# Optimization experiments

Measured on AMD Instinct MI355X. Metric: run time of the kernel, lower is better.

Reference implementation:

```python
import jax, jax.numpy as jnp
import numpy as np

B, QH, QW = 16, 64, 64
KH, KW = 64, 64
H, D, DK, K, S = 8, 256, 32, 4, 1


def setup_inputs() -> dict:
    key = jax.random.key(0)
    ks = jax.random.split(key, 16)
    def lin(i, din, dout, wscale=1.0):
        w = jax.random.normal(ks[i], (din, dout), jnp.float32) * (wscale / np.sqrt(din))
        b = jax.random.normal(ks[i + 1], (dout,), jnp.float32) * 0.02
        return w, b
    Wq, bq = lin(0, D, D)
    Wb, bb = lin(2, D, D)
    Wk, bk = lin(4, D, D)
    Woff, boff = lin(6, D, 2 * H * K * S, wscale=0.1)  # small offsets keep samples near ref point
    WA, bA = lin(8, D, H * K * S)
    Wm, bm = lin(10, D, D)
    return dict(
        query=jax.random.normal(ks[12], (B, QH, QW, D), jnp.float32),
        keys=jax.random.normal(ks[13], (B, KH, KW, D), jnp.float32),
        ref_point=jax.random.uniform(ks[14], (B, QH, QW, 2), jnp.float32),
        src_query=jax.random.normal(ks[15], (B, QH, QW, D), jnp.float32),
        Wq=Wq, bq=bq, Wb=Wb, bb=bb, Wk=Wk, bk=bk,
        Woff=Woff, boff=boff, WA=WA, bA=bA, Wm=Wm, bm=bm)


def _bilinear_zeros(img, px, py):
    # img [N, Hs, Ws, C]; px, py pixel coords [N, K, QH, QW]
    # Matches torch F.grid_sample(mode='bilinear', padding_mode='zeros'):
    # each out-of-bounds corner contributes zero.
    N, Hs, Ws, _ = img.shape
    x0 = jnp.floor(px); y0 = jnp.floor(py)
    wx1 = px - x0; wy1 = py - y0
    n = jnp.arange(N)[:, None, None, None]
    def corner(xf, yf, w):
        xi = xf.astype(jnp.int32); yi = yf.astype(jnp.int32)
        valid = (xi >= 0) & (xi < Ws) & (yi >= 0) & (yi < Hs)
        v = img[n, jnp.clip(yi, 0, Hs - 1), jnp.clip(xi, 0, Ws - 1)]
        return v * (w * valid)[..., None]
    return (corner(x0, y0, (1 - wx1) * (1 - wy1)) + corner(x0 + 1, y0, wx1 * (1 - wy1))
            + corner(x0, y0 + 1, (1 - wx1) * wy1) + corner(x0 + 1, y0 + 1, wx1 * wy1))


def reference(query, keys, ref_point, src_query, Wq, bq, Wb, bb, Wk, bk,
              Woff, boff, WA, bA, Wm, bm):
    _ = query @ Wq + bq  # q_proj output is computed but unused in the original forward
    sq = src_query @ Wb + bb
    off = (sq @ Woff + boff).reshape(B, QH, QW, H, S, K, 2)
    off = off.transpose(0, 3, 4, 5, 1, 2, 6).reshape(B * H, S, K, QH, QW, 2)
    A = jax.nn.softmax((sq @ WA + bA).reshape(B, QH, QW, H, S * K), axis=-1)
    A = A.transpose(0, 3, 1, 2, 4).reshape(B * H, QH, QW, S, K)
    # k_proj on the (single-scale) key feature map -> per-head maps [B*H, KH, KW, DK]
    kf = (keys @ Wk + bk).reshape(B, KH, KW, H, DK).transpose(0, 3, 1, 2, 4).reshape(B * H, KH, KW, DK)
    # restore_scale then torch .repeat(h,1,1,1): flat index n -> batch n % B (faithful to original)
    rr = ref_point * jnp.array([KW - 1, KH - 1], jnp.float32)
    rr = jnp.tile(rr, (H, 1, 1, 1))  # [B*H, QH, QW, 2]
    samples = []
    for l in range(S):
        pts = rr[:, None] + off[:, l]                 # [B*H, K, QH, QW, 2]
        vgx = 2.0 * pts[..., 0] / max(KW - 1, 1) - 1.0
        vgy = 2.0 * pts[..., 1] / max(KH - 1, 1) - 1.0
        px = ((vgx + 1.0) * KW - 1.0) / 2.0           # grid_sample align_corners=False unnormalize
        py = ((vgy + 1.0) * KH - 1.0) / 2.0
        samples.append(_bilinear_zeros(kf, px, py))   # [B*H, K, QH, QW, DK]
    samp = jnp.stack(samples, axis=1)                 # [B*H, S, K, QH, QW, DK]
    feat = jnp.einsum('nskhwd,nhwsk->nhwd', samp, A)  # weighted sum over scales*points
    feat = feat.reshape(B, H, QH, QW, DK).transpose(0, 2, 3, 1, 4).reshape(B, QH, QW, D)
    return feat @ Wm + bm
```

## Files before the change

kernel.cpp:

```cpp
#include <hip/hip_runtime.h>
#include <hip/hip_bf16.h>

using bf16 = __hip_bfloat16;
typedef short bf16x8 __attribute__((ext_vector_type(8)));
typedef float f32x4 __attribute__((ext_vector_type(4)));

#define DD 256
#define MTOT 65536

static __device__ __forceinline__ short f2bs(float f) {
    bf16 h = __float2bfloat16(f);
    return *reinterpret_cast<short*>(&h);
}
static __device__ __forceinline__ float bs2f(short s) {
    unsigned u = (unsigned)(unsigned short)s << 16;
    return __uint_as_float(u);
}

static __device__ __forceinline__ void gll16(const void* g, void* l) {
    __builtin_amdgcn_global_load_lds(
        (const __attribute__((address_space(1))) unsigned int*)g,
        (__attribute__((address_space(3))) unsigned int*)l, 16, 0, 0);
}

static __device__ __forceinline__ int swz_idx(int n, int k) {
    return n * 256 + ((((k >> 3) ^ (n & 7)) << 3) | (k & 7));
}

__global__ __launch_bounds__(256) void k_transpose(
    const float* __restrict__ Wb, const float* __restrict__ Wk, const float* __restrict__ Wm,
    const float* __restrict__ Woff, const float* __restrict__ WA,
    bf16* __restrict__ WbT, bf16* __restrict__ WkT, bf16* __restrict__ WmT,
    bf16* __restrict__ WoffAT)
{
    int idx = blockIdx.x * 256 + threadIdx.x;
    if (idx < 3 * 65536) {
        int which = idx >> 16, e = idx & 65535;
        int i = e >> 8, j = e & 255;
        const float* src = which == 0 ? Wb : (which == 1 ? Wk : Wm);
        bf16*        dst = which == 0 ? WbT : (which == 1 ? WkT : WmT);
        dst[swz_idx(j, i)] = __float2bfloat16(src[e]);
    } else {
        int e = idx - 3 * 65536;
        if (e < 96 * 256) {
            int j = e >> 8, i = e & 255;
            WoffAT[swz_idx(j, i)] = __float2bfloat16((j < 64) ? Woff[i * 64 + j]
                                                              : WA[i * 32 + (j - 64)]);
        }
    }
}

template <int NTW, int NCOLS, bool AF32>
static __device__ __forceinline__ void gemm_lds2(
    const void* __restrict__ Av, const bf16* __restrict__ BTswz,
    bf16* __restrict__ Bs, char* __restrict__ As,
    int row0, int tid, f32x4 (&acc)[2][NTW])
{
    const int wave = tid >> 6, lane = tid & 63;
    const int rg = wave >> 1, cg = wave & 1;
    const int rsub = lane & 15, kg = lane >> 4;
    constexpr int SB = NCOLS / 32;
    constexpr int SA = AF32 ? 4 : 2;
    constexpr int ABYTES = AF32 ? 16384 : 8192;

    auto stageB = [&](int s) {
#pragma unroll
        for (int i = 0; i < SB; ++i) {
            int cc = wave * SB + i;
            int i16 = cc * 64 + lane;
            int n = i16 >> 3, lg = i16 & 7;
            gll16(BTswz + (size_t)n * 256 + s * 64 + lg * 8, (char*)Bs + (size_t)i16 * 16);
        }
    };
    auto stageA = [&](int s, int buf) {
#pragma unroll
        for (int i = 0; i < SA; ++i) {
            if constexpr (AF32) {
                int cc = wave * 4 + i;
                int row = cc * 4 + (lane >> 4);
                int g = (lane & 15) ^ (row & 15);
                gll16((const float*)Av + (size_t)(row0 + row) * DD + s * 64 + g * 4,
                      As + (size_t)buf * ABYTES + cc * 1024 + lane * 16);
            } else {
                int cc = wave * 2 + i;
                int row = cc * 8 + (lane >> 3);
                int g = (lane & 7) ^ (row & 7);
                gll16((const bf16*)Av + (size_t)(row0 + row) * DD + s * 64 + g * 8,
                      As + (size_t)buf * ABYTES + cc * 1024 + lane * 16);
            }
        }
    };

    stageA(0, 0);
    int cur = 0;
#pragma unroll
    for (int s = 0; s < 4; ++s) {
        stageB(s);
        if (s < 3) {
            stageA(s + 1, cur ^ 1);
            asm volatile("s_waitcnt vmcnt(%0)" :: "i"(SA) : "memory");
        } else {
            asm volatile("s_waitcnt vmcnt(0)" ::: "memory");
        }
        __builtin_amdgcn_s_barrier();
#pragma unroll
        for (int kkl = 0; kkl < 2; ++kkl) {
            bf16x8 afr[2];
#pragma unroll
            for (int st = 0; st < 2; ++st) {
                int row = rg * 32 + st * 16 + rsub;
                if constexpr (AF32) {
                    const char* base = As + cur * ABYTES + row * 256;
                    int G0 = kkl * 8 + kg * 2;
                    f32x4 v0 = *(const f32x4*)(base + ((G0 ^ (row & 15)) << 4));
                    f32x4 v1 = *(const f32x4*)(base + (((G0 + 1) ^ (row & 15)) << 4));
                    bf16x8 a;
#pragma unroll
                    for (int e = 0; e < 4; ++e) { a[e] = f2bs(v0[e]); a[e + 4] = f2bs(v1[e]); }
                    afr[st] = a;
                } else {
                    const char* base = As + cur * ABYTES + row * 128;
                    int g = kkl * 4 + kg;
                    afr[st] = *(const bf16x8*)(base + ((g ^ (row & 7)) << 4));
                }
            }
            int lg = kkl * 4 + kg;
#pragma unroll
            for (int nt = 0; nt < NTW; ++nt) {
                int n = cg * (NTW * 16) + nt * 16 + rsub;
                bf16x8 b = *(const bf16x8*)((const char*)Bs + (size_t)n * 128 + ((lg ^ (n & 7)) << 4));
                acc[0][nt] = __builtin_amdgcn_mfma_f32_16x16x32_bf16(afr[0], b, acc[0][nt], 0, 0, 0);
                acc[1][nt] = __builtin_amdgcn_mfma_f32_16x16x32_bf16(afr[1], b, acc[1][nt], 0, 0, 0);
            }
        }
        asm volatile("s_waitcnt lgkmcnt(0)" ::: "memory");
        __builtin_amdgcn_s_barrier();
        cur ^= 1;
    }
}

__global__ __launch_bounds__(256) void k_gemm_sqoffA(
    const float* __restrict__ src, const bf16* __restrict__ WbT, const float* __restrict__ bb,
    const bf16* __restrict__ WoffAT, const float* __restrict__ boff, const float* __restrict__ bA,
    float* __restrict__ off_ws, float* __restrict__ A_ws)
{
    __shared__ __align__(16) bf16 Bs[256 * 64];
    __shared__ __align__(16) char As[2 * 16384];
    int tid = threadIdx.x, lane = tid & 63, wave = tid >> 6;
    int row0 = blockIdx.x * 64;
    f32x4 acc[2][8] = {};
    gemm_lds2<8, 256, true>(src, WbT, Bs, As, row0, tid, acc);

    {
        int col = lane & 15;
        int jbase = (wave & 1) * 128;
        int lrb = (wave >> 1) * 32 + ((lane >> 4) << 2);
#pragma unroll
        for (int mt = 0; mt < 2; ++mt)
#pragma unroll
            for (int nt = 0; nt < 8; ++nt) {
                int j = jbase + nt * 16 + col;
                float bias = bb[j];
                int g = j >> 3;
#pragma unroll
                for (int r = 0; r < 4; ++r) {
                    int lr = lrb + mt * 16 + r;
                    *(short*)(As + lr * 512 + (((g ^ (lr & 7)) << 4)) + (j & 7) * 2) =
                        f2bs(acc[mt][nt][r] + bias);
                }
            }
    }
    __syncthreads();

    f32x4 acc2[2][3] = {};
    const int rsub = lane & 15, kg = lane >> 4;
    const int rg = wave >> 1, cg2 = wave & 1;
    auto stageOB = [&](int s, int buf) {
#pragma unroll
        for (int i = 0; i < 3; ++i) {
            int i16 = (wave * 3 + i) * 64 + lane;
            int n = i16 >> 3, lg = i16 & 7;
            gll16(WoffAT + (size_t)n * 256 + s * 64 + lg * 8,
                  (char*)Bs + buf * 12288 + (size_t)i16 * 16);
        }
    };
    stageOB(0, 0);
    int cur = 0;
#pragma unroll
    for (int s = 0; s < 4; ++s) {
        if (s < 3) {
            stageOB(s + 1, cur ^ 1);
            asm volatile("s_waitcnt vmcnt(3)" ::: "memory");
        } else {
            asm volatile("s_waitcnt vmcnt(0)" ::: "memory");
        }
        __builtin_amdgcn_s_barrier();
#pragma unroll
        for (int kkl = 0; kkl < 2; ++kkl) {
            bf16x8 afr[2];
#pragma unroll
            for (int st = 0; st < 2; ++st) {
                int lr = rg * 32 + st * 16 + rsub;
                int g = s * 8 + kkl * 4 + kg;
                afr[st] = *(const bf16x8*)(As + lr * 512 + ((g ^ (lr & 7)) << 4));
            }
            int lg = kkl * 4 + kg;
#pragma unroll
            for (int nt = 0; nt < 3; ++nt) {
                int n = cg2 * 48 + nt * 16 + rsub;
                bf16x8 b = *(const bf16x8*)((const char*)Bs + cur * 12288 + (size_t)n * 128
                                            + ((lg ^ (n & 7)) << 4));
                acc2[0][nt] = __builtin_amdgcn_mfma_f32_16x16x32_bf16(afr[0], b, acc2[0][nt], 0, 0, 0);
                acc2[1][nt] = __builtin_amdgcn_mfma_f32_16x16x32_bf16(afr[1], b, acc2[1][nt], 0, 0, 0);
            }
        }
        asm volatile("s_waitcnt lgkmcnt(0)" ::: "memory");
        __builtin_amdgcn_s_barrier();
        cur ^= 1;
    }
    int col = lane & 15;
    int jbase = cg2 * 48;
    int rb = row0 + rg * 32 + ((lane >> 4) << 2);
#pragma unroll
    for (int mt = 0; mt < 2; ++mt) {
#pragma unroll
        for (int nt = 0; nt < 3; ++nt) {
            int j = jbase + nt * 16 + col;
            if (j < 64) {
                float bias = boff[j];
#pragma unroll
                for (int r = 0; r < 4; ++r) {
                    int m = rb + mt * 16 + r;
                    off_ws[(size_t)m * 64 + j] = acc2[mt][nt][r] + bias;
                }
            } else {
                int ac = j - 64;
                float bias = bA[ac];
#pragma unroll
                for (int r = 0; r < 4; ++r) {
                    int m = rb + mt * 16 + r;
                    float v  = acc2[mt][nt][r] + bias;
                    float mx = fmaxf(v, __shfl_xor(v, 1));
                    mx       = fmaxf(mx, __shfl_xor(mx, 2));
                    float e  = __expf(v - mx);
                    float su = e + __shfl_xor(e, 1);
                    su      += __shfl_xor(su, 2);
                    A_ws[(size_t)m * 32 + ac] = e / su;
                }
            }
        }
    }
}

__global__ __launch_bounds__(256) void k_gemm_kf(
    const float* __restrict__ keys, const bf16* __restrict__ WkT,
    const float* __restrict__ bk, bf16* __restrict__ kf)
{
    __shared__ __align__(16) bf16 Bs[256 * 64];
    __shared__ __align__(16) char As[2 * 16384];
    int tid = threadIdx.x, lane = tid & 63, wave = tid >> 6;
    int row0 = blockIdx.x * 64;
    f32x4 acc[2][8] = {};
    gemm_lds2<8, 256, true>(keys, WkT, Bs, As, row0, tid, acc);
    int col = lane & 15;
    int jbase = (wave & 1) * 128;
    int rb = row0 + (wave >> 1) * 32 + ((lane >> 4) << 2);
#pragma unroll
    for (int mt = 0; mt < 2; ++mt)
#pragma unroll
        for (int nt = 0; nt < 8; ++nt) {
            int j = jbase + nt * 16 + col;
            float bias = bk[j];
#pragma unroll
            for (int r = 0; r < 4; ++r) {
                int m = rb + mt * 16 + r;
                size_t dst = (((size_t)(m >> 12) * 8 + (j >> 5)) * 4096 + (m & 4095)) * 32 + (j & 31);
                kf[dst] = __float2bfloat16(acc[mt][nt][r] + bias);
            }
        }
}

__global__ __launch_bounds__(256) void k_sample(
    const float* __restrict__ ref_point, const float* __restrict__ off_ws,
    const float* __restrict__ A_ws, const bf16* __restrict__ kf,
    bf16* __restrict__ feat)
{
    int bid = blockIdx.x;
    int xcd = bid & 7, within = bid >> 3;
    int bb_ = xcd * 2 + (within >> 9);
    int pixblk = within & 511;
    int t  = threadIdx.x;
    int q  = t >> 5;
    int h  = (t >> 2) & 7;
    int cg = t & 3;
    int m  = (bb_ << 12) + pixblk * 8 + q;
    int b  = bb_, pix = m & 4095;
    int rbatch = (b * 8 + h) & 15;
    const float* rp = ref_point + ((size_t)rbatch * 4096 + pix) * 2;
    float rx = rp[0] * 63.0f;
    float ry = rp[1] * 63.0f;
    const bf16* kfh = kf + ((size_t)(b * 8 + h) * 4096) * 32 + cg * 8;
    float acc[8] = {};
#pragma unroll
    for (int k = 0; k < 4; ++k) {
        const float* op = off_ws + (size_t)m * 64 + (h * 4 + k) * 2;
        float ox = op[0], oy = op[1];
        float a  = A_ws[(size_t)m * 32 + h * 4 + k];
        float px = (rx + ox) * (64.0f / 63.0f) - 0.5f;
        float py = (ry + oy) * (64.0f / 63.0f) - 0.5f;
        float x0 = floorf(px), y0 = floorf(py);
        float wx1 = px - x0, wy1 = py - y0;
        int xi = (int)x0, yi = (int)y0;
        float ax0 = (1.f - wx1) * ((xi     >= 0 && xi     < 64) ? 1.f : 0.f);
        float ax1 = wx1         * ((xi + 1 >= 0 && xi + 1 < 64) ? 1.f : 0.f);
        float ay0 = (1.f - wy1) * ((yi     >= 0 && yi     < 64) ? a : 0.f);
        float ay1 = wy1         * ((yi + 1 >= 0 && yi + 1 < 64) ? a : 0.f);
        int xc0 = min(max(xi, 0), 63),      xc1 = min(max(xi + 1, 0), 63);
        int yc0 = min(max(yi, 0), 63) * 64, yc1 = min(max(yi + 1, 0), 63) * 64;
        bf16x8 v00 = *(const bf16x8*)(kfh + (yc0 + xc0) * 32);
        bf16x8 v01 = *(const bf16x8*)(kfh + (yc0 + xc1) * 32);
        bf16x8 v10 = *(const bf16x8*)(kfh + (yc1 + xc0) * 32);
        bf16x8 v11 = *(const bf16x8*)(kfh + (yc1 + xc1) * 32);
        float w00 = ax0 * ay0, w01 = ax1 * ay0, w10 = ax0 * ay1, w11 = ax1 * ay1;
#pragma unroll
        for (int e = 0; e < 8; ++e) {
            acc[e] += w00 * bs2f(v00[e]) + w01 * bs2f(v01[e])
                    + w10 * bs2f(v10[e]) + w11 * bs2f(v11[e]);
        }
    }
    bf16x8 o;
#pragma unroll
    for (int e = 0; e < 8; ++e) o[e] = f2bs(acc[e]);
    *(bf16x8*)(feat + (size_t)m * DD + h * 32 + cg * 8) = o;
}

__global__ __launch_bounds__(256) void k_gemm_out(
    const bf16* __restrict__ feat, const bf16* __restrict__ WmT,
    const float* __restrict__ bm, float* __restrict__ out)
{
    __shared__ __align__(16) bf16 Bs[256 * 64];
    __shared__ __align__(16) char As[2 * 8192];
    int tid = threadIdx.x, lane = tid & 63, wave = tid >> 6;
    int row0 = blockIdx.x * 64;
    f32x4 acc[2][8] = {};
    gemm_lds2<8, 256, false>(feat, WmT, Bs, As, row0, tid, acc);
    int col = lane & 15;
    int jbase = (wave & 1) * 128;
    int rb = row0 + (wave >> 1) * 32 + ((lane >> 4) << 2);
#pragma unroll
    for (int mt = 0; mt < 2; ++mt)
#pragma unroll
        for (int nt = 0; nt < 8; ++nt) {
            int j = jbase + nt * 16 + col;
            float bias = bm[j];
#pragma unroll
            for (int r = 0; r < 4; ++r)
                out[(size_t)(rb + mt * 16 + r) * DD + j] =
                    acc[mt][nt][r] + bias;
        }
}

extern "C" void kernel_launch(void* const* d_in, const int* in_sizes, int n_in,
                              void* d_out, int out_size, void* d_ws, size_t ws_size,
                              hipStream_t stream)
{
    (void)in_sizes; (void)n_in; (void)out_size; (void)ws_size;
    const float* keys = (const float*)d_in[1];
    const float* refp = (const float*)d_in[2];
    const float* srcq = (const float*)d_in[3];
    const float* Wb   = (const float*)d_in[6];
    const float* bb   = (const float*)d_in[7];
    const float* Wk   = (const float*)d_in[8];
    const float* bk   = (const float*)d_in[9];
    const float* Woff = (const float*)d_in[10];
    const float* boff = (const float*)d_in[11];
    const float* WA   = (const float*)d_in[12];
    const float* bA   = (const float*)d_in[13];
    const float* Wm   = (const float*)d_in[14];
    const float* bm   = (const float*)d_in[15];

    char* ws = (char*)d_ws;
    bf16*  WbT    = (bf16*)(ws + 0);
    bf16*  WkT    = (bf16*)(ws + 131072);
    bf16*  WmT    = (bf16*)(ws + 262144);
    bf16*  WoffAT = (bf16*)(ws + 393216);
    bf16*  kf_ws  = (bf16*)(ws + 442368 + 33554432ull);
    bf16*  feat_ws= (bf16*)(ws + 442368 + 2ull * 33554432ull);
    float* off_ws = (float*)(ws + 442368 + 3ull * 33554432ull);
    float* A_ws   = (float*)(ws + 442368 + 3ull * 33554432ull + 16777216ull);

    float* out = (float*)d_out;

    k_transpose  <<<864, 256, 0, stream>>>(Wb, Wk, Wm, Woff, WA, WbT, WkT, WmT, WoffAT);
    k_gemm_sqoffA<<<1024, 256, 0, stream>>>(srcq, WbT, bb, WoffAT, boff, bA, off_ws, A_ws);
    k_gemm_kf    <<<1024, 256, 0, stream>>>(keys, WkT, bk, kf_ws);
    k_sample     <<<8192, 256, 0, stream>>>(refp, off_ws, A_ws, kf_ws, feat_ws);
    k_gemm_out   <<<1024, 256, 0, stream>>>(feat_ws, WmT, bm, out);
}
```

Baseline: 122.6 us.

## Fuse sampling into output GEMM and merge the two projection GEMMs

Merges the sq/off/A GEMM and the key-projection GEMM into one launch, with interleaved blocks dispatched by block-index parity over shared LDS. Fuses bilinear sampling with the output projection: each block samples 64 rows straight into a swizzled LDS A-tile, then runs the MFMA GEMM against Wm. This drops the feat workspace round-trip and two launches. In exchange the sample stage now runs with 1024 blocks instead of 8192, which lowers latency hiding for the gather loads, and 64KB of LDS per block may limit occupancy.

```diff
diff --git a/kernel.cpp b/kernel.cpp
--- a/kernel.cpp
+++ b/kernel.cpp
@@ -139,15 +139,16 @@
     }
 }
 
-__global__ __launch_bounds__(256) void k_gemm_sqoffA(
+static __device__ void body_sqoffA(
+    int bid, char* smem,
     const float* __restrict__ src, const bf16* __restrict__ WbT, const float* __restrict__ bb,
     const bf16* __restrict__ WoffAT, const float* __restrict__ boff, const float* __restrict__ bA,
     float* __restrict__ off_ws, float* __restrict__ A_ws)
 {
-    __shared__ __align__(16) bf16 Bs[256 * 64];
-    __shared__ __align__(16) char As[2 * 16384];
+    bf16* Bs = (bf16*)smem;
+    char* As = smem + 32768;
     int tid = threadIdx.x, lane = tid & 63, wave = tid >> 6;
-    int row0 = blockIdx.x * 64;
+    int row0 = bid * 64;
     f32x4 acc[2][8] = {};
     gemm_lds2<8, 256, true>(src, WbT, Bs, As, row0, tid, acc);
 
@@ -252,14 +253,15 @@
     }
 }
 
-__global__ __launch_bounds__(256) void k_gemm_kf(
+static __device__ void body_kf(
+    int bid, char* smem,
     const float* __restrict__ keys, const bf16* __restrict__ WkT,
     const float* __restrict__ bk, bf16* __restrict__ kf)
 {
-    __shared__ __align__(16) bf16 Bs[256 * 64];
-    __shared__ __align__(16) char As[2 * 16384];
+    bf16* Bs = (bf16*)smem;
+    char* As = smem + 32768;
     int tid = threadIdx.x, lane = tid & 63, wave = tid >> 6;
-    int row0 = blockIdx.x * 64;
+    int row0 = bid * 64;
     f32x4 acc[2][8] = {};
     gemm_lds2<8, 256, true>(keys, WkT, Bs, As, row0, tid, acc);
     int col = lane & 15;
@@ -280,73 +282,121 @@
         }
 }
 
-__global__ __launch_bounds__(256) void k_sample(
+__global__ __launch_bounds__(256) void k_fusedA(
+    const float* __restrict__ src, const bf16* __restrict__ WbT, const float* __restrict__ bb,
+    const bf16* __restrict__ WoffAT, const float* __restrict__ boff, const float* __restrict__ bA,
+    float* __restrict__ off_ws, float* __restrict__ A_ws,
+    const float* __restrict__ keys, const bf16* __restrict__ WkT,
+    const float* __restrict__ bk, bf16* __restrict__ kf)
+{
+    __shared__ __align__(16) char smem[65536];
+    int bid = blockIdx.x;
+    if (bid & 1)
+        body_kf(bid >> 1, smem, keys, WkT, bk, kf);
+    else
+        body_sqoffA(bid >> 1, smem, src, WbT, bb, WoffAT, boff, bA, off_ws, A_ws);
+}
+
+__global__ __launch_bounds__(256) void k_sample_out(
     const float* __restrict__ ref_point, const float* __restrict__ off_ws,
     const float* __restrict__ A_ws, const bf16* __restrict__ kf,
-    bf16* __restrict__ feat)
-{
-    int bid = blockIdx.x;
-    int xcd = bid & 7, within = bid >> 3;
-    int bb_ = xcd * 2 + (within >> 9);
-    int pixblk = within & 511;
-    int t  = threadIdx.x;
-    int q  = t >> 5;
-    int h  = (t >> 2) & 7;
-    int cg = t & 3;
-    int m  = (bb_ << 12) + pixblk * 8 + q;
-    int b  = bb_, pix = m & 4095;
-    int rbatch = (b * 8 + h) & 15;
-    const float* rp = ref_point + ((size_t)rbatch * 4096 + pix) * 2;
-    float rx = rp[0] * 63.0f;
-    float ry = rp[1] * 63.0f;
-    const bf16* kfh = kf + ((size_t)(b * 8 + h) * 4096) * 32 + cg * 8;
-    float acc[8] = {};
-#pragma unroll
-    for (int k = 0; k < 4; ++k) {
-        const float* op = off_ws + (size_t)m * 64 + (h * 4 + k) * 2;
-        float ox = op[0], oy = op[1];
-        float a  = A_ws[(size_t)m * 32 + h * 4 + k];
-        float px = (rx + ox) * (64.0f / 63.0f) - 0.5f;
-        float py = (ry + oy) * (64.0f / 63.0f) - 0.5f;
-        float x0 = floorf(px), y0 = floorf(py);
-        float wx1 = px - x0, wy1 = py - y0;
-        int xi = (int)x0, yi = (int)y0;
-        float ax0 = (1.f - wx1) * ((xi     >= 0 && xi     < 64) ? 1.f : 0.f);
-        float ax1 = wx1         * ((xi + 1 >= 0 && xi + 1 < 64) ? 1.f : 0.f);
-        float ay0 = (1.f - wy1) * ((yi     >= 0 && yi     < 64) ? a : 0.f);
-        float ay1 = wy1         * ((yi + 1 >= 0 && yi + 1 < 64) ? a : 0.f);
-        int xc0 = min(max(xi, 0), 63),      xc1 = min(max(xi + 1, 0), 63);
-        int yc0 = min(max(yi, 0), 63) * 64, yc1 = min(max(yi + 1, 0), 63) * 64;
-        bf16x8 v00 = *(const bf16x8*)(kfh + (yc0 + xc0) * 32);
-        bf16x8 v01 = *(const bf16x8*)(kfh + (yc0 + xc1) * 32);
-        bf16x8 v10 = *(const bf16x8*)(kfh + (yc1 + xc0) * 32);
-        bf16x8 v11 = *(const bf16x8*)(kfh + (yc1 + xc1) * 32);
-        float w00 = ax0 * ay0, w01 = ax1 * ay0, w10 = ax0 * ay1, w11 = ax1 * ay1;
-#pragma unroll
-        for (int e = 0; e < 8; ++e) {
-            acc[e] += w00 * bs2f(v00[e]) + w01 * bs2f(v01[e])
-                    + w10 * bs2f(v10[e]) + w11 * bs2f(v11[e]);
-        }
-    }
-    bf16x8 o;
-#pragma unroll
-    for (int e = 0; e < 8; ++e) o[e] = f2bs(acc[e]);
-    *(bf16x8*)(feat + (size_t)m * DD + h * 32 + cg * 8) = o;
-}
-
-__global__ __launch_bounds__(256) void k_gemm_out(
-    const bf16* __restrict__ feat, const bf16* __restrict__ WmT,
-    const float* __restrict__ bm, float* __restrict__ out)
-{
-    __shared__ __align__(16) bf16 Bs[256 * 64];
-    __shared__ __align__(16) char As[2 * 8192];
-    int tid = threadIdx.x, lane = tid & 63, wave = tid >> 6;
+    const bf16* __restrict__ WmT, const float* __restrict__ bm,
+    float* __restrict__ out)
+{
+    __shared__ __align__(16) char smem[65536];
+    bf16* Bs = (bf16*)smem;
+    char* As = smem + 32768;
+    int tid = threadIdx.x;
     int row0 = blockIdx.x * 64;
-    f32x4 acc[2][8] = {};
-    gemm_lds2<8, 256, false>(feat, WmT, Bs, As, row0, tid, acc);
+    int q  = tid >> 5;
+    int h  = (tid >> 2) & 7;
+    int cg = tid & 3;
+    int jcol = h * 32 + cg * 8;
+    int gcol = jcol >> 3;
+
+#pragma unroll 2
+    for (int qq = 0; qq < 8; ++qq) {
+        int lr = qq * 8 + q;
+        int m  = row0 + lr;
+        int b  = m >> 12, pix = m & 4095;
+        int rbatch = (b * 8 + h) & 15;
+        const float* rp = ref_point + ((size_t)rbatch * 4096 + pix) * 2;
+        float rx = rp[0] * 63.0f;
+        float ry = rp[1] * 63.0f;
+        const bf16* kfh = kf + ((size_t)(b * 8 + h) * 4096) * 32 + cg * 8;
+        float acc[8] = {};
+#pragma unroll
+        for (int k = 0; k < 4; ++k) {
+            const float* op = off_ws + (size_t)m * 64 + (h * 4 + k) * 2;
+            float ox = op[0], oy = op[1];
+            float a  = A_ws[(size_t)m * 32 + h * 4 + k];
+            float px = (rx + ox) * (64.0f / 63.0f) - 0.5f;
+            float py = (ry + oy) * (64.0f / 63.0f) - 0.5f;
+            float x0 = floorf(px), y0 = floorf(py);
+            float wx1 = px - x0, wy1 = py - y0;
+            int xi = (int)x0, yi = (int)y0;
+            float ax0 = (1.f - wx1) * ((xi     >= 0 && xi     < 64) ? 1.f : 0.f);
+            float ax1 = wx1         * ((xi + 1 >= 0 && xi + 1 < 64) ? 1.f : 0.f);
+            float ay0 = (1.f - wy1) * ((yi     >= 0 && yi     < 64) ? a : 0.f);
+            float ay1 = wy1         * ((yi + 1 >= 0 && yi + 1 < 64) ? a : 0.f);
+            int xc0 = min(max(xi, 0), 63),      xc1 = min(max(xi + 1, 0), 63);
+            int yc0 = min(max(yi, 0), 63) * 64, yc1 = min(max(yi + 1, 0), 63) * 64;
+            bf16x8 v00 = *(const bf16x8*)(kfh + (yc0 + xc0) * 32);
+            bf16x8 v01 = *(const bf16x8*)(kfh + (yc0 + xc1) * 32);
+            bf16x8 v10 = *(const bf16x8*)(kfh + (yc1 + xc0) * 32);
+            bf16x8 v11 = *(const bf16x8*)(kfh + (yc1 + xc1) * 32);
+            float w00 = ax0 * ay0, w01 = ax1 * ay0, w10 = ax0 * ay1, w11 = ax1 * ay1;
+#pragma unroll
+            for (int e = 0; e < 8; ++e) {
+                acc[e] += w00 * bs2f(v00[e]) + w01 * bs2f(v01[e])
+                        + w10 * bs2f(v10[e]) + w11 * bs2f(v11[e]);
+            }
+        }
+        bf16x8 o;
+#pragma unroll
+        for (int e = 0; e < 8; ++e) o[e] = f2bs(acc[e]);
+        *(bf16x8*)(As + lr * 512 + ((gcol ^ (lr & 7)) << 4)) = o;
+    }
+    __syncthreads();
+
+    f32x4 acc2[2][8] = {};
+    int lane = tid & 63, wave = tid >> 6;
+    const int rsub = lane & 15, kg = lane >> 4;
+    const int rg = wave >> 1, cgw = wave & 1;
+#pragma unroll
+    for (int s = 0; s < 4; ++s) {
+#pragma unroll
+        for (int i = 0; i < 8; ++i) {
+            int i16 = (wave * 8 + i) * 64 + lane;
+            int n = i16 >> 3, lg = i16 & 7;
+            gll16(WmT + (size_t)n * 256 + s * 64 + lg * 8, (char*)Bs + (size_t)i16 * 16);
+        }
+        asm volatile("s_waitcnt vmcnt(0)" ::: "memory");
+        __builtin_amdgcn_s_barrier();
+#pragma unroll
+        for (int kkl = 0; kkl < 2; ++kkl) {
+            bf16x8 afr[2];
+#pragma unroll
+            for (int st = 0; st < 2; ++st) {
+                int lr = rg * 32 + st * 16 + rsub;
+                int g = s * 8 + kkl * 4 + kg;
+                afr[st] = *(const bf16x8*)(As + lr * 512 + ((g ^ (lr & 7)) << 4));
+            }
+            int lg = kkl * 4 + kg;
+#pragma unroll
+            for (int nt = 0; nt < 8; ++nt) {
+                int n = cgw * 128 + nt * 16 + rsub;
+                bf16x8 b = *(const bf16x8*)((const char*)Bs + (size_t)n * 128 + ((lg ^ (n & 7)) << 4));
+                acc2[0][nt] = __builtin_amdgcn_mfma_f32_16x16x32_bf16(afr[0], b, acc2[0][nt], 0, 0, 0);
+                acc2[1][nt] = __builtin_amdgcn_mfma_f32_16x16x32_bf16(afr[1], b, acc2[1][nt], 0, 0, 0);
+            }
+        }
+        asm volatile("s_waitcnt lgkmcnt(0)" ::: "memory");
+        __builtin_amdgcn_s_barrier();
+    }
     int col = lane & 15;
-    int jbase = (wave & 1) * 128;
-    int rb = row0 + (wave >> 1) * 32 + ((lane >> 4) << 2);
+    int jbase = cgw * 128;
+    int rb = row0 + rg * 32 + ((lane >> 4) << 2);
 #pragma unroll
     for (int mt = 0; mt < 2; ++mt)
 #pragma unroll
@@ -356,7 +406,7 @@
 #pragma unroll
             for (int r = 0; r < 4; ++r)
                 out[(size_t)(rb + mt * 16 + r) * DD + j] =
-                    acc[mt][nt][r] + bias;
+                    acc2[mt][nt][r] + bias;
         }
 }
 
@@ -385,15 +435,13 @@
     bf16*  WmT    = (bf16*)(ws + 262144);
     bf16*  WoffAT = (bf16*)(ws + 393216);
     bf16*  kf_ws  = (bf16*)(ws + 442368 + 33554432ull);
-    bf16*  feat_ws= (bf16*)(ws + 442368 + 2ull * 33554432ull);
     float* off_ws = (float*)(ws + 442368 + 3ull * 33554432ull);
     float* A_ws   = (float*)(ws + 442368 + 3ull * 33554432ull + 16777216ull);
 
     float* out = (float*)d_out;
 
-    k_transpose  <<<864, 256, 0, stream>>>(Wb, Wk, Wm, Woff, WA, WbT, WkT, WmT, WoffAT);
-    k_gemm_sqoffA<<<1024, 256, 0, stream>>>(srcq, WbT, bb, WoffAT, boff, bA, off_ws, A_ws);
-    k_gemm_kf    <<<1024, 256, 0, stream>>>(keys, WkT, bk, kf_ws);
-    k_sample     <<<8192, 256, 0, stream>>>(refp, off_ws, A_ws, kf_ws, feat_ws);
-    k_gemm_out   <<<1024, 256, 0, stream>>>(feat_ws, WmT, bm, out);
-}
+    k_transpose <<<864, 256, 0, stream>>>(Wb, Wk, Wm, Woff, WA, WbT, WkT, WmT, WoffAT);
+    k_fusedA    <<<2048, 256, 0, stream>>>(srcq, WbT, bb, WoffAT, boff, bA, off_ws, A_ws,
+                                           keys, WkT, bk, kf_ws);
+    k_sample_out<<<1024, 256, 0, stream>>>(refp, off_ws, A_ws, kf_ws, WmT, bm, out);
+}
```

New measurement: 129.3 us. 1.06x slower.
